# Optimization experiments

Hardware: AMD Instinct MI355X
Metric: run time of the kernel (lower is better)

The kernel has to match this reference:

```python
import jax, jax.numpy as jnp
import numpy as np

N_NODES = 100000


def gcn_conv(x, edge_index, W, b):
    """PyG-style GCNConv: add self-loops, symmetric deg^{-1/2} normalization,
    then scatter-sum of transformed source features into targets."""
    n = x.shape[0]
    loops = jnp.arange(n, dtype=edge_index.dtype)
    row = jnp.concatenate([edge_index[0], loops])  # source
    col = jnp.concatenate([edge_index[1], loops])  # target
    deg = jax.ops.segment_sum(jnp.ones_like(col, dtype=x.dtype), col, num_segments=n)
    dinv = jnp.where(deg > 0, jax.lax.rsqrt(deg), 0.0)
    norm = dinv[row] * dinv[col]  # [E+N]
    h = x @ W  # [N, out]
    msg = h[row] * norm[:, None]  # gather + scale, [E+N, out]
    out = jax.ops.segment_sum(msg, col, num_segments=n)
    return out + b


def setup_inputs() -> dict:
    key = jax.random.key(0)
    k1, k2, k3, k4, k5 = jax.random.split(key, 5)
    x = jax.random.normal(k1, (N_NODES, 972), dtype=jnp.float32)
    edge_index = jax.random.randint(k2, (2, 1600000), 0, N_NODES, dtype=jnp.int64)
    edge_label_index = jax.random.randint(k3, (2, 1000000), 0, N_NODES, dtype=jnp.int64)
    W1 = jax.random.normal(k4, (384, 128), dtype=jnp.float32) * (1.0 / np.sqrt(384))
    b1 = jnp.zeros((128,), dtype=jnp.float32)
    W2 = jax.random.normal(k5, (128, 64), dtype=jnp.float32) * (1.0 / np.sqrt(128))
    b2 = jnp.zeros((64,), dtype=jnp.float32)
    return {"x": x, "edge_index": edge_index, "edge_label_index": edge_label_index,
            "W1": W1, "b1": b1, "W2": W2, "b2": b2}


def reference(x, edge_index, edge_label_index, W1, b1, W2, b2):
    # encode: slice features, two GCN layers with relu between
    h = x[:, 588:]  # [N, 384]
    h = jax.nn.relu(gcn_conv(h, edge_index, W1, b1))
    z = gcn_conv(h, edge_index, W2, b2)  # [N, 64]
    # decode: gather-dot-sum over labeled edges
    logits = jnp.sum(z[edge_label_index[0]] * z[edge_label_index[1]], axis=-1)
    return logits
```

## Files before the change

### kernel.cpp

```cpp
#include <hip/hip_runtime.h>
#include <hip/hip_bf16.h>

#define N_NODES 100000
#define N_EDGES 1600000
#define N_LBL   1000000
#define XC 972
#define XO 588
#define D1 128
#define D2 64

typedef float f32x4 __attribute__((ext_vector_type(4)));
typedef short bf16x8 __attribute__((ext_vector_type(8)));

__device__ inline unsigned f2bf(float f) {
    unsigned u = __float_as_uint(f);
    return (u + 0x7fffu + ((u >> 16) & 1u)) >> 16;
}
__device__ inline float bf_lo(unsigned v) { return __uint_as_float(v << 16); }
__device__ inline float bf_hi(unsigned v) { return __uint_as_float(v & 0xffff0000u); }

__device__ inline unsigned pack_bf2(float lo, float hi) {
    union { __hip_bfloat162 h; unsigned u; } p;
    p.h = __float22bfloat162_rn(make_float2(lo, hi));
    return p.u;
}
__device__ inline bf16x8 to_bf8(float4 a, float4 b) {
    union { __hip_bfloat162 h[4]; bf16x8 v; } u;
    u.h[0] = __float22bfloat162_rn(make_float2(a.x, a.y));
    u.h[1] = __float22bfloat162_rn(make_float2(a.z, a.w));
    u.h[2] = __float22bfloat162_rn(make_float2(b.x, b.y));
    u.h[3] = __float22bfloat162_rn(make_float2(b.z, b.w));
    return u.v;
}
__device__ inline void add8(float (&a)[8], uint4 u) {
    a[0] += bf_lo(u.x); a[1] += bf_hi(u.x);
    a[2] += bf_lo(u.y); a[3] += bf_hi(u.y);
    a[4] += bf_lo(u.z); a[5] += bf_hi(u.z);
    a[6] += bf_lo(u.w); a[7] += bf_hi(u.w);
}

__global__ __launch_bounds__(256) void k_place_prep(const int* __restrict__ row,
                                                    const int* __restrict__ col,
                                                    unsigned* __restrict__ cursor,
                                                    int* __restrict__ srcidx,
                                                    const float* __restrict__ W1,
                                                    const float* __restrict__ W2,
                                                    unsigned short* __restrict__ w1p,
                                                    unsigned short* __restrict__ w2p) {
    if (blockIdx.x < N_EDGES / 256) {
        int e = blockIdx.x * 256 + threadIdx.x;
        int c = col[e];
        unsigned j = atomicAdd(&cursor[c], 1u);
        srcidx[((size_t)c << 6) + j] = row[e];
    } else {
        int i = (blockIdx.x - N_EDGES / 256) * 256 + threadIdx.x;
        if (i < 49152) {
            int j = i & 7, lane = (i >> 3) & 63, nt = (i >> 9) & 7, ks = i >> 12;
            int k = ks * 32 + ((lane >> 4) << 3) + j;
            int n = (nt << 4) + (lane & 15);
            w1p[i] = (unsigned short)f2bf(W1[k * D1 + n]);
        } else {
            int t = i - 49152;
            int j = t & 7, lane = (t >> 3) & 63, nt = (t >> 9) & 3, ks = t >> 11;
            int k = ks * 32 + ((lane >> 4) << 3) + j;
            int n = (nt << 4) + (lane & 15);
            w2p[t] = (unsigned short)f2bf(W2[k * D2 + n]);
        }
    }
}

__global__ __launch_bounds__(256) void k_gemm1(const float* __restrict__ x,
                                               const unsigned short* __restrict__ w1p,
                                               const unsigned* __restrict__ deg,
                                               unsigned short* __restrict__ s1) {
    const int lane = threadIdx.x & 63;
    const int wid  = threadIdx.x >> 6;
    const int lrow = lane & 15;
    const int kq   = lane >> 4;

    const int row0 = blockIdx.x * 64 + wid * 16;
    const int rc = min(row0 + lrow, N_NODES - 1);
    const float* pA = x + (size_t)rc * XC + XO + (kq << 3);

    f32x4 acc[8];
#pragma unroll
    for (int t = 0; t < 8; ++t) acc[t] = (f32x4)0.f;

#pragma unroll 2
    for (int ks = 0; ks < 12; ++ks) {
        float4 a0 = *reinterpret_cast<const float4*>(pA + ks * 32);
        float4 a1 = *reinterpret_cast<const float4*>(pA + ks * 32 + 4);
        bf16x8 aA = to_bf8(a0, a1);
#pragma unroll
        for (int t = 0; t < 8; ++t) {
            bf16x8 bf = *reinterpret_cast<const bf16x8*>(
                w1p + ((size_t)((ks * 8 + t) * 64 + lane) << 3));
            acc[t] = __builtin_amdgcn_mfma_f32_16x16x32_bf16(aA, bf, acc[t], 0, 0, 0);
        }
    }

    const int rowq = row0 + kq * 4;
#pragma unroll
    for (int r = 0; r < 4; ++r) {
        int rw = rowq + r;
        if (rw < N_NODES) {
            float d = rsqrtf((float)(deg[rw] + 1u));
#pragma unroll
            for (int t = 0; t < 8; ++t)
                s1[(size_t)rw * D1 + lrow + t * 16] =
                    (unsigned short)f2bf(acc[t][r] * d);
        }
    }
}

__global__ __launch_bounds__(256) void k_fused(const unsigned short* __restrict__ s1,
                                               const int* __restrict__ srcidx,
                                               const unsigned* __restrict__ deg,
                                               const float* __restrict__ b1,
                                               const unsigned short* __restrict__ w2p,
                                               unsigned short* __restrict__ s2) {
    const int lane = threadIdx.x & 63;
    const int wid  = threadIdx.x >> 6;
    const int n    = lane & 15;
    const int kq   = lane >> 4;
    const int base = blockIdx.x * 64 + wid * 16;
    const int c  = base + n;
    const int cc = min(c, N_NODES - 1);

    float acc[4][8];
    const unsigned short* srow = s1 + (size_t)cc * D1 + (kq << 3);
    {
        uint4 u0 = *reinterpret_cast<const uint4*>(srow);
        uint4 u1 = *reinterpret_cast<const uint4*>(srow + 32);
        uint4 u2 = *reinterpret_cast<const uint4*>(srow + 64);
        uint4 u3 = *reinterpret_cast<const uint4*>(srow + 96);
#pragma unroll
        for (int j = 0; j < 8; ++j) { acc[0][j] = 0.f; acc[1][j] = 0.f;
                                      acc[2][j] = 0.f; acc[3][j] = 0.f; }
        add8(acc[0], u0); add8(acc[1], u1); add8(acc[2], u2); add8(acc[3], u3);
    }
    const int cnt = (int)deg[cc];
    const int* sp = srcidx + ((size_t)cc << 6);
    int rn = (cnt > 0) ? sp[0] : 0;
    for (int j = 0; j < cnt; ++j) {
        int r = rn;
        if (j + 1 < cnt) rn = sp[j + 1];
        const unsigned short* rr = s1 + (size_t)r * D1 + (kq << 3);
        uint4 u0 = *reinterpret_cast<const uint4*>(rr);
        uint4 u1 = *reinterpret_cast<const uint4*>(rr + 32);
        uint4 u2 = *reinterpret_cast<const uint4*>(rr + 64);
        uint4 u3 = *reinterpret_cast<const uint4*>(rr + 96);
        add8(acc[0], u0); add8(acc[1], u1); add8(acc[2], u2); add8(acc[3], u3);
    }

    const float d = rsqrtf((float)(cnt + 1));
    bf16x8 af[4];
#pragma unroll
    for (int p = 0; p < 4; ++p) {
        const float* bp = b1 + p * 32 + (kq << 3);
        float4 ba = *reinterpret_cast<const float4*>(bp);
        float4 bb = *reinterpret_cast<const float4*>(bp + 4);
        float4 h0 = make_float4(fmaxf(fmaf(acc[p][0], d, ba.x), 0.f),
                                fmaxf(fmaf(acc[p][1], d, ba.y), 0.f),
                                fmaxf(fmaf(acc[p][2], d, ba.z), 0.f),
                                fmaxf(fmaf(acc[p][3], d, ba.w), 0.f));
        float4 h1 = make_float4(fmaxf(fmaf(acc[p][4], d, bb.x), 0.f),
                                fmaxf(fmaf(acc[p][5], d, bb.y), 0.f),
                                fmaxf(fmaf(acc[p][6], d, bb.z), 0.f),
                                fmaxf(fmaf(acc[p][7], d, bb.w), 0.f));
        af[p] = to_bf8(h0, h1);
    }

    f32x4 acc2[4];
#pragma unroll
    for (int nt = 0; nt < 4; ++nt) acc2[nt] = (f32x4)0.f;
#pragma unroll
    for (int ks = 0; ks < 4; ++ks)
#pragma unroll
        for (int nt = 0; nt < 4; ++nt) {
            bf16x8 bf = *reinterpret_cast<const bf16x8*>(
                w2p + ((size_t)((ks * 4 + nt) * 64 + lane) << 3));
            acc2[nt] = __builtin_amdgcn_mfma_f32_16x16x32_bf16(af[ks], bf, acc2[nt], 0, 0, 0);
        }

#pragma unroll
    for (int r = 0; r < 4; ++r) {
        int rw = base + kq * 4 + r;
        if (rw < N_NODES) {
            float dm = rsqrtf((float)(deg[rw] + 1u));
#pragma unroll
            for (int nt = 0; nt < 4; ++nt)
                s2[(size_t)rw * D2 + nt * 16 + n] =
                    (unsigned short)f2bf(acc2[nt][r] * dm);
        }
    }
}

__global__ __launch_bounds__(256) void k_gather2(const unsigned short* __restrict__ s2,
                                                 const int* __restrict__ srcidx,
                                                 const unsigned* __restrict__ deg,
                                                 const float* __restrict__ b,
                                                 uint4* __restrict__ zv) {
    const int c    = blockIdx.x * 32 + (threadIdx.x >> 3);
    const int l8   = threadIdx.x & 7;

    float a[8];
#pragma unroll
    for (int j = 0; j < 8; ++j) a[j] = 0.f;
    add8(a, *reinterpret_cast<const uint4*>(s2 + (size_t)c * D2 + (l8 << 3)));

    const int cnt = (int)deg[c];
    const int* sp = srcidx + ((size_t)c << 6);
    int rn = (cnt > 0) ? sp[0] : 0;
    for (int j = 0; j < cnt; ++j) {
        int r = rn;
        if (j + 1 < cnt) rn = sp[j + 1];
        add8(a, *reinterpret_cast<const uint4*>(s2 + (size_t)r * D2 + (l8 << 3)));
    }
    const float d = rsqrtf((float)(cnt + 1));
    const float4 b0 = reinterpret_cast<const float4*>(b)[l8 * 2];
    const float4 b1v = reinterpret_cast<const float4*>(b)[l8 * 2 + 1];
    uint4 o;
    o.x = pack_bf2(fmaf(a[0], d, b0.x),  fmaf(a[1], d, b0.y));
    o.y = pack_bf2(fmaf(a[2], d, b0.z),  fmaf(a[3], d, b0.w));
    o.z = pack_bf2(fmaf(a[4], d, b1v.x), fmaf(a[5], d, b1v.y));
    o.w = pack_bf2(fmaf(a[6], d, b1v.z), fmaf(a[7], d, b1v.w));
    zv[(size_t)c * 8 + l8] = o;
}

__global__ __launch_bounds__(256) void k_score(const int4* __restrict__ Z,
                                               const int* __restrict__ ea,
                                               const int* __restrict__ eb,
                                               float* __restrict__ out) {
    int tid = blockIdx.x * 256 + threadIdx.x;
    int e = tid >> 3;
    int l = tid & 7;
    int u = ea[e], v = eb[e];
    int4 a = Z[(size_t)u * 8 + l];
    int4 c = Z[(size_t)v * 8 + l];
    float p = bf_lo(a.x) * bf_lo(c.x) + bf_hi(a.x) * bf_hi(c.x)
            + bf_lo(a.y) * bf_lo(c.y) + bf_hi(a.y) * bf_hi(c.y)
            + bf_lo(a.z) * bf_lo(c.z) + bf_hi(a.z) * bf_hi(c.z)
            + bf_lo(a.w) * bf_lo(c.w) + bf_hi(a.w) * bf_hi(c.w);
    p += __shfl_down(p, 4, 8);
    p += __shfl_down(p, 2, 8);
    p += __shfl_down(p, 1, 8);
    if (l == 0) out[e] = p;
}

extern "C" void kernel_launch(void* const* d_in, const int* in_sizes, int n_in,
                              void* d_out, int out_size, void* d_ws, size_t ws_size,
                              hipStream_t stream) {
    const float* x   = (const float*)d_in[0];
    const int*   ei  = (const int*)d_in[1];
    const int*   eli = (const int*)d_in[2];
    const float* W1  = (const float*)d_in[3];
    const float* b1  = (const float*)d_in[4];
    const float* W2  = (const float*)d_in[5];
    const float* b2  = (const float*)d_in[6];
    float* out = (float*)d_out;

    char* ws = (char*)d_ws;
    unsigned*       cursor = (unsigned*)(ws + 0);
    unsigned short* w1p    = (unsigned short*)(ws + 400000);
    unsigned short* w2p    = (unsigned short*)(ws + 498304);
    int*            srcidx = (int*)(ws + 514688);
    unsigned short* s1     = (unsigned short*)(ws + 26114688);
    unsigned short* s2     = (unsigned short*)(ws + 51714688);
    unsigned short* z      = (unsigned short*)(ws + 64514688);

    hipMemsetAsync(cursor, 0, 400000, stream);
    k_place_prep<<<N_EDGES / 256 + 224, 256, 0, stream>>>(ei, ei + N_EDGES, cursor,
                                                          srcidx, W1, W2, w1p, w2p);
    k_gemm1  <<<(N_NODES + 63) / 64, 256, 0, stream>>>(x, w1p, cursor, s1);
    k_fused  <<<(N_NODES + 63) / 64, 256, 0, stream>>>(s1, srcidx, cursor, b1, w2p, s2);
    k_gather2<<<N_NODES / 32, 256, 0, stream>>>(s2, srcidx, cursor, b2, (uint4*)z);
    k_score  <<<(size_t)N_LBL * 8 / 256, 256, 0, stream>>>((const int4*)z, eli,
                                                           eli + N_LBL, out);
}
```

Measured before the change: 321.3 us.

## Fuse GEMM1 with edge placement and move source degree scaling into gather

The memset is replaced by zeroing the cursor inside the weight-prep kernel. GEMM1 and the atomic edge-placement pass now run as one launch, so the dense matmul and the scatter can overlap. This works because GEMM1 no longer scales by source degree. The per-source deg^{-1/2} is applied during the first-layer gather, which adds a random degree load per edge. Both gather loops also load indices vectorised and are unrolled by 2 or 4 to keep more loads in flight.

```diff
diff --git a/kernel.cpp b/kernel.cpp
--- a/kernel.cpp
+++ b/kernel.cpp
@@ -8,6 +8,8 @@
 #define XO 588
 #define D1 128
 #define D2 64
+#define GEMM1_BLOCKS ((N_NODES + 63) / 64)
+#define PLACE_BLOCKS (N_EDGES / 256)
 
 typedef float f32x4 __attribute__((ext_vector_type(4)));
 typedef short bf16x8 __attribute__((ext_vector_type(8)));
@@ -38,78 +40,84 @@
     a[4] += bf_lo(u.z); a[5] += bf_hi(u.z);
     a[6] += bf_lo(u.w); a[7] += bf_hi(u.w);
 }
-
-__global__ __launch_bounds__(256) void k_place_prep(const int* __restrict__ row,
-                                                    const int* __restrict__ col,
-                                                    unsigned* __restrict__ cursor,
-                                                    int* __restrict__ srcidx,
-                                                    const float* __restrict__ W1,
-                                                    const float* __restrict__ W2,
-                                                    unsigned short* __restrict__ w1p,
-                                                    unsigned short* __restrict__ w2p) {
-    if (blockIdx.x < N_EDGES / 256) {
-        int e = blockIdx.x * 256 + threadIdx.x;
-        int c = col[e];
+__device__ inline void fma8(float (&a)[8], uint4 u, float s) {
+    a[0] = fmaf(bf_lo(u.x), s, a[0]); a[1] = fmaf(bf_hi(u.x), s, a[1]);
+    a[2] = fmaf(bf_lo(u.y), s, a[2]); a[3] = fmaf(bf_hi(u.y), s, a[3]);
+    a[4] = fmaf(bf_lo(u.z), s, a[4]); a[5] = fmaf(bf_hi(u.z), s, a[5]);
+    a[6] = fmaf(bf_lo(u.w), s, a[6]); a[7] = fmaf(bf_hi(u.w), s, a[7]);
+}
+
+__global__ __launch_bounds__(256) void k_prep(const float* __restrict__ W1,
+                                              const float* __restrict__ W2,
+                                              unsigned short* __restrict__ w1p,
+                                              unsigned short* __restrict__ w2p,
+                                              unsigned* __restrict__ cursor) {
+    int i = blockIdx.x * 256 + threadIdx.x;
+    if (i < N_NODES) cursor[i] = 0u;
+    if (i < 49152) {
+        int j = i & 7, lane = (i >> 3) & 63, nt = (i >> 9) & 7, ks = i >> 12;
+        int k = ks * 32 + ((lane >> 4) << 3) + j;
+        int n = (nt << 4) + (lane & 15);
+        w1p[i] = (unsigned short)f2bf(W1[k * D1 + n]);
+    } else if (i < 57344) {
+        int t = i - 49152;
+        int j = t & 7, lane = (t >> 3) & 63, nt = (t >> 9) & 3, ks = t >> 11;
+        int k = ks * 32 + ((lane >> 4) << 3) + j;
+        int n = (nt << 4) + (lane & 15);
+        w2p[t] = (unsigned short)f2bf(W2[k * D2 + n]);
+    }
+}
+
+__global__ __launch_bounds__(256) void k_mega(const float* __restrict__ x,
+                                              const unsigned short* __restrict__ w1p,
+                                              unsigned short* __restrict__ s1,
+                                              const int* __restrict__ erow,
+                                              const int* __restrict__ ecol,
+                                              unsigned* __restrict__ cursor,
+                                              int* __restrict__ srcidx) {
+    if (blockIdx.x < GEMM1_BLOCKS) {
+        const int lane = threadIdx.x & 63;
+        const int wid  = threadIdx.x >> 6;
+        const int lrow = lane & 15;
+        const int kq   = lane >> 4;
+
+        const int row0 = blockIdx.x * 64 + wid * 16;
+        const int rc = min(row0 + lrow, N_NODES - 1);
+        const float* pA = x + (size_t)rc * XC + XO + (kq << 3);
+
+        f32x4 acc[8];
+#pragma unroll
+        for (int t = 0; t < 8; ++t) acc[t] = (f32x4)0.f;
+
+#pragma unroll 2
+        for (int ks = 0; ks < 12; ++ks) {
+            float4 a0 = *reinterpret_cast<const float4*>(pA + ks * 32);
+            float4 a1 = *reinterpret_cast<const float4*>(pA + ks * 32 + 4);
+            bf16x8 aA = to_bf8(a0, a1);
+#pragma unroll
+            for (int t = 0; t < 8; ++t) {
+                bf16x8 bf = *reinterpret_cast<const bf16x8*>(
+                    w1p + ((size_t)((ks * 8 + t) * 64 + lane) << 3));
+                acc[t] = __builtin_amdgcn_mfma_f32_16x16x32_bf16(aA, bf, acc[t], 0, 0, 0);
+            }
+        }
+
+        const int rowq = row0 + kq * 4;
+#pragma unroll
+        for (int r = 0; r < 4; ++r) {
+            int rw = rowq + r;
+            if (rw < N_NODES) {
+#pragma unroll
+                for (int t = 0; t < 8; ++t)
+                    s1[(size_t)rw * D1 + lrow + t * 16] =
+                        (unsigned short)f2bf(acc[t][r]);
+            }
+        }
+    } else {
+        int e = (blockIdx.x - GEMM1_BLOCKS) * 256 + threadIdx.x;
+        int c = ecol[e];
         unsigned j = atomicAdd(&cursor[c], 1u);
-        srcidx[((size_t)c << 6) + j] = row[e];
-    } else {
-        int i = (blockIdx.x - N_EDGES / 256) * 256 + threadIdx.x;
-        if (i < 49152) {
-            int j = i & 7, lane = (i >> 3) & 63, nt = (i >> 9) & 7, ks = i >> 12;
-            int k = ks * 32 + ((lane >> 4) << 3) + j;
-            int n = (nt << 4) + (lane & 15);
-            w1p[i] = (unsigned short)f2bf(W1[k * D1 + n]);
-        } else {
-            int t = i - 49152;
-            int j = t & 7, lane = (t >> 3) & 63, nt = (t >> 9) & 3, ks = t >> 11;
-            int k = ks * 32 + ((lane >> 4) << 3) + j;
-            int n = (nt << 4) + (lane & 15);
-            w2p[t] = (unsigned short)f2bf(W2[k * D2 + n]);
-        }
-    }
-}
-
-__global__ __launch_bounds__(256) void k_gemm1(const float* __restrict__ x,
-                                               const unsigned short* __restrict__ w1p,
-                                               const unsigned* __restrict__ deg,
-                                               unsigned short* __restrict__ s1) {
-    const int lane = threadIdx.x & 63;
-    const int wid  = threadIdx.x >> 6;
-    const int lrow = lane & 15;
-    const int kq   = lane >> 4;
-
-    const int row0 = blockIdx.x * 64 + wid * 16;
-    const int rc = min(row0 + lrow, N_NODES - 1);
-    const float* pA = x + (size_t)rc * XC + XO + (kq << 3);
-
-    f32x4 acc[8];
-#pragma unroll
-    for (int t = 0; t < 8; ++t) acc[t] = (f32x4)0.f;
-
-#pragma unroll 2
-    for (int ks = 0; ks < 12; ++ks) {
-        float4 a0 = *reinterpret_cast<const float4*>(pA + ks * 32);
-        float4 a1 = *reinterpret_cast<const float4*>(pA + ks * 32 + 4);
-        bf16x8 aA = to_bf8(a0, a1);
-#pragma unroll
-        for (int t = 0; t < 8; ++t) {
-            bf16x8 bf = *reinterpret_cast<const bf16x8*>(
-                w1p + ((size_t)((ks * 8 + t) * 64 + lane) << 3));
-            acc[t] = __builtin_amdgcn_mfma_f32_16x16x32_bf16(aA, bf, acc[t], 0, 0, 0);
-        }
-    }
-
-    const int rowq = row0 + kq * 4;
-#pragma unroll
-    for (int r = 0; r < 4; ++r) {
-        int rw = rowq + r;
-        if (rw < N_NODES) {
-            float d = rsqrtf((float)(deg[rw] + 1u));
-#pragma unroll
-            for (int t = 0; t < 8; ++t)
-                s1[(size_t)rw * D1 + lrow + t * 16] =
-                    (unsigned short)f2bf(acc[t][r] * d);
-        }
+        srcidx[((size_t)c << 6) + j] = erow[e];
     }
 }
 
@@ -127,47 +135,68 @@
     const int c  = base + n;
     const int cc = min(c, N_NODES - 1);
 
+    const int cnt = (int)deg[cc];
+    const float dc = rsqrtf((float)(cnt + 1));
+
     float acc[4][8];
-    const unsigned short* srow = s1 + (size_t)cc * D1 + (kq << 3);
+#pragma unroll
+    for (int p = 0; p < 4; ++p)
+#pragma unroll
+        for (int j = 0; j < 8; ++j) acc[p][j] = 0.f;
+
     {
-        uint4 u0 = *reinterpret_cast<const uint4*>(srow);
-        uint4 u1 = *reinterpret_cast<const uint4*>(srow + 32);
-        uint4 u2 = *reinterpret_cast<const uint4*>(srow + 64);
-        uint4 u3 = *reinterpret_cast<const uint4*>(srow + 96);
-#pragma unroll
-        for (int j = 0; j < 8; ++j) { acc[0][j] = 0.f; acc[1][j] = 0.f;
-                                      acc[2][j] = 0.f; acc[3][j] = 0.f; }
-        add8(acc[0], u0); add8(acc[1], u1); add8(acc[2], u2); add8(acc[3], u3);
-    }
-    const int cnt = (int)deg[cc];
+        const unsigned short* srow = s1 + (size_t)cc * D1 + (kq << 3);
+        fma8(acc[0], *reinterpret_cast<const uint4*>(srow),      dc);
+        fma8(acc[1], *reinterpret_cast<const uint4*>(srow + 32), dc);
+        fma8(acc[2], *reinterpret_cast<const uint4*>(srow + 64), dc);
+        fma8(acc[3], *reinterpret_cast<const uint4*>(srow + 96), dc);
+    }
+
     const int* sp = srcidx + ((size_t)cc << 6);
-    int rn = (cnt > 0) ? sp[0] : 0;
-    for (int j = 0; j < cnt; ++j) {
-        int r = rn;
-        if (j + 1 < cnt) rn = sp[j + 1];
+    int j = 0;
+    for (; j + 2 <= cnt; j += 2) {
+        int2 idx = *reinterpret_cast<const int2*>(sp + j);
+        float d0 = rsqrtf((float)(deg[idx.x] + 1u));
+        float d1 = rsqrtf((float)(deg[idx.y] + 1u));
+        const unsigned short* r0 = s1 + (size_t)idx.x * D1 + (kq << 3);
+        const unsigned short* r1 = s1 + (size_t)idx.y * D1 + (kq << 3);
+        uint4 a0 = *reinterpret_cast<const uint4*>(r0);
+        uint4 a1 = *reinterpret_cast<const uint4*>(r0 + 32);
+        uint4 a2 = *reinterpret_cast<const uint4*>(r0 + 64);
+        uint4 a3 = *reinterpret_cast<const uint4*>(r0 + 96);
+        uint4 c0 = *reinterpret_cast<const uint4*>(r1);
+        uint4 c1 = *reinterpret_cast<const uint4*>(r1 + 32);
+        uint4 c2 = *reinterpret_cast<const uint4*>(r1 + 64);
+        uint4 c3 = *reinterpret_cast<const uint4*>(r1 + 96);
+        fma8(acc[0], a0, d0); fma8(acc[1], a1, d0);
+        fma8(acc[2], a2, d0); fma8(acc[3], a3, d0);
+        fma8(acc[0], c0, d1); fma8(acc[1], c1, d1);
+        fma8(acc[2], c2, d1); fma8(acc[3], c3, d1);
+    }
+    if (j < cnt) {
+        int r = sp[j];
+        float dr = rsqrtf((float)(deg[r] + 1u));
         const unsigned short* rr = s1 + (size_t)r * D1 + (kq << 3);
-        uint4 u0 = *reinterpret_cast<const uint4*>(rr);
-        uint4 u1 = *reinterpret_cast<const uint4*>(rr + 32);
-        uint4 u2 = *reinterpret_cast<const uint4*>(rr + 64);
-        uint4 u3 = *reinterpret_cast<const uint4*>(rr + 96);
-        add8(acc[0], u0); add8(acc[1], u1); add8(acc[2], u2); add8(acc[3], u3);
-    }
-
-    const float d = rsqrtf((float)(cnt + 1));
+        fma8(acc[0], *reinterpret_cast<const uint4*>(rr),      dr);
+        fma8(acc[1], *reinterpret_cast<const uint4*>(rr + 32), dr);
+        fma8(acc[2], *reinterpret_cast<const uint4*>(rr + 64), dr);
+        fma8(acc[3], *reinterpret_cast<const uint4*>(rr + 96), dr);
+    }
+
     bf16x8 af[4];
 #pragma unroll
     for (int p = 0; p < 4; ++p) {
         const float* bp = b1 + p * 32 + (kq << 3);
         float4 ba = *reinterpret_cast<const float4*>(bp);
         float4 bb = *reinterpret_cast<const float4*>(bp + 4);
-        float4 h0 = make_float4(fmaxf(fmaf(acc[p][0], d, ba.x), 0.f),
-                                fmaxf(fmaf(acc[p][1], d, ba.y), 0.f),
-                                fmaxf(fmaf(acc[p][2], d, ba.z), 0.f),
-                                fmaxf(fmaf(acc[p][3], d, ba.w), 0.f));
-        float4 h1 = make_float4(fmaxf(fmaf(acc[p][4], d, bb.x), 0.f),
-                                fmaxf(fmaf(acc[p][5], d, bb.y), 0.f),
-                                fmaxf(fmaf(acc[p][6], d, bb.z), 0.f),
-                                fmaxf(fmaf(acc[p][7], d, bb.w), 0.f));
+        float4 h0 = make_float4(fmaxf(fmaf(acc[p][0], dc, ba.x), 0.f),
+                                fmaxf(fmaf(acc[p][1], dc, ba.y), 0.f),
+                                fmaxf(fmaf(acc[p][2], dc, ba.z), 0.f),
+                                fmaxf(fmaf(acc[p][3], dc, ba.w), 0.f));
+        float4 h1 = make_float4(fmaxf(fmaf(acc[p][4], dc, bb.x), 0.f),
+                                fmaxf(fmaf(acc[p][5], dc, bb.y), 0.f),
+                                fmaxf(fmaf(acc[p][6], dc, bb.z), 0.f),
+                                fmaxf(fmaf(acc[p][7], dc, bb.w), 0.f));
         af[p] = to_bf8(h0, h1);
     }
 
@@ -211,10 +240,17 @@
 
     const int cnt = (int)deg[c];
     const int* sp = srcidx + ((size_t)c << 6);
-    int rn = (cnt > 0) ? sp[0] : 0;
-    for (int j = 0; j < cnt; ++j) {
-        int r = rn;
-        if (j + 1 < cnt) rn = sp[j + 1];
+    int j = 0;
+    for (; j + 4 <= cnt; j += 4) {
+        int4 idx = *reinterpret_cast<const int4*>(sp + j);
+        uint4 u0 = *reinterpret_cast<const uint4*>(s2 + (size_t)idx.x * D2 + (l8 << 3));
+        uint4 u1 = *reinterpret_cast<const uint4*>(s2 + (size_t)idx.y * D2 + (l8 << 3));
+        uint4 u2 = *reinterpret_cast<const uint4*>(s2 + (size_t)idx.z * D2 + (l8 << 3));
+        uint4 u3 = *reinterpret_cast<const uint4*>(s2 + (size_t)idx.w * D2 + (l8 << 3));
+        add8(a, u0); add8(a, u1); add8(a, u2); add8(a, u3);
+    }
+    for (; j < cnt; ++j) {
+        int r = sp[j];
         add8(a, *reinterpret_cast<const uint4*>(s2 + (size_t)r * D2 + (l8 << 3)));
     }
     const float d = rsqrtf((float)(cnt + 1));
@@ -269,10 +305,9 @@
     unsigned short* s2     = (unsigned short*)(ws + 51714688);
     unsigned short* z      = (unsigned short*)(ws + 64514688);
 
-    hipMemsetAsync(cursor, 0, 400000, stream);
-    k_place_prep<<<N_EDGES / 256 + 224, 256, 0, stream>>>(ei, ei + N_EDGES, cursor,
-                                                          srcidx, W1, W2, w1p, w2p);
-    k_gemm1  <<<(N_NODES + 63) / 64, 256, 0, stream>>>(x, w1p, cursor, s1);
+    k_prep   <<<392, 256, 0, stream>>>(W1, W2, w1p, w2p, cursor);
+    k_mega   <<<GEMM1_BLOCKS + PLACE_BLOCKS, 256, 0, stream>>>(x, w1p, s1, ei,
+                                                               ei + N_EDGES, cursor, srcidx);
     k_fused  <<<(N_NODES + 63) / 64, 256, 0, stream>>>(s1, srcidx, cursor, b1, w2p, s2);
     k_gather2<<<N_NODES / 32, 256, 0, stream>>>(s2, srcidx, cursor, b2, (uint4*)z);
     k_score  <<<(size_t)N_LBL * 8 / 256, 256, 0, stream>>>((const int4*)z, eli,
```

Measured after the change: 277.4 us. -13.7%, faster.
